# Performance work log

Hardware: AMD Instinct MI355X
Metric: run time of the kernel (lower is better)

## Reference

```python
import jax, jax.numpy as jnp
import numpy as np
from jax import lax

NHEAD = 8
EPS = 1e-5
B, T, DIN, DOUT = 32, 64, 512, 128
FF_ENC, FF_DEC, NLAYERS = 64, 16, 4


def _ln(x, g, b):
    mu = jnp.mean(x, -1, keepdims=True)
    var = jnp.mean(jnp.square(x - mu), -1, keepdims=True)
    return (x - mu) * lax.rsqrt(var + EPS) * g + b


def _lin(x, w, b):
    return x @ w.T + b


def _mha(q_in, kv_in, qkv_w, qkv_b, out_w, out_b):
    # PyTorch MultiheadAttention (batch_first, eval mode -> no dropout)
    b_, sq, d = q_in.shape
    sk = kv_in.shape[1]
    dh = d // NHEAD
    wq, wk, wv = jnp.split(qkv_w, 3, axis=0)
    bq, bk, bv = jnp.split(qkv_b, 3, axis=0)
    q = _lin(q_in, wq, bq).reshape(b_, sq, NHEAD, dh)
    k = _lin(kv_in, wk, bk).reshape(b_, sk, NHEAD, dh)
    v = _lin(kv_in, wv, bv).reshape(b_, sk, NHEAD, dh)
    s = jnp.einsum('bqhd,bkhd->bhqk', q, k) * (1.0 / np.sqrt(dh))
    a = jax.nn.softmax(s, axis=-1)
    o = jnp.einsum('bhqk,bkhd->bqhd', a, v).reshape(b_, sq, d)
    return _lin(o, out_w, out_b)


def _enc_layer(x, p):
    (qkv_w, qkv_b, ow, ob, f1w, f1b, f2w, f2b, g1, b1, g2, b2) = p
    # post-norm (norm_first=False), relu activation, dropout off (eval)
    x = _ln(x + _mha(x, x, qkv_w, qkv_b, ow, ob), g1, b1)
    ff = _lin(jax.nn.relu(_lin(x, f1w, f1b)), f2w, f2b)
    return _ln(x + ff, g2, b2)


def _dec_layer(tgt, mem, dp):
    (sqkv_w, sqkv_b, sow, sob, cqkv_w, cqkv_b, cow, cob,
     f1w, f1b, f2w, f2b, g1, b1, g2, b2, g3, b3) = dp
    x = _ln(tgt + _mha(tgt, tgt, sqkv_w, sqkv_b, sow, sob), g1, b1)  # no mask, as in source
    x = _ln(x + _mha(x, mem, cqkv_w, cqkv_b, cow, cob), g2, b2)
    ff = _lin(jax.nn.relu(_lin(x, f1w, f1b)), f2w, f2b)
    return _ln(x + ff, g3, b3)


def _forward(src, enc_qkv_w, enc_qkv_b, enc_out_w, enc_out_b,
             enc_ff1_w, enc_ff1_b, enc_ff2_w, enc_ff2_b,
             enc_ln1_g, enc_ln1_b, enc_ln2_g, enc_ln2_b,
             fc_w, fc_b,
             dec_sa_qkv_w, dec_sa_qkv_b, dec_sa_out_w, dec_sa_out_b,
             dec_ca_qkv_w, dec_ca_qkv_b, dec_ca_out_w, dec_ca_out_b,
             dec_ff1_w, dec_ff1_b, dec_ff2_w, dec_ff2_b,
             dec_ln1_g, dec_ln1_b, dec_ln2_g, dec_ln2_b, dec_ln3_g, dec_ln3_b):
    mem = src
    for i in range(NLAYERS):
        p = (enc_qkv_w[i], enc_qkv_b[i], enc_out_w[i], enc_out_b[i],
             enc_ff1_w[i], enc_ff1_b[i], enc_ff2_w[i], enc_ff2_b[i],
             enc_ln1_g[i], enc_ln1_b[i], enc_ln2_g[i], enc_ln2_b[i])
        mem = _enc_layer(mem, p)
    mem = _lin(mem, fc_w, fc_b)  # [B, T, DOUT]
    dp = (dec_sa_qkv_w, dec_sa_qkv_b, dec_sa_out_w, dec_sa_out_b,
          dec_ca_qkv_w, dec_ca_qkv_b, dec_ca_out_w, dec_ca_out_b,
          dec_ff1_w, dec_ff1_b, dec_ff2_w, dec_ff2_b,
          dec_ln1_g, dec_ln1_b, dec_ln2_g, dec_ln2_b, dec_ln3_g, dec_ln3_b)

    def step(tgt, t):
        out = _dec_layer(tgt, mem, dp)           # full decoder pass over padded tgt
        row = lax.dynamic_slice_in_dim(out, t, 1, axis=1)
        tgt = lax.dynamic_update_slice_in_dim(tgt, row, t + 1, axis=1)
        return tgt, None

    tgt0 = jnp.zeros((src.shape[0], T + 1, DOUT), src.dtype)
    tgt, _ = lax.scan(step, tgt0, jnp.arange(T))
    return tgt[:, 1:]


def setup_inputs() -> dict:
    key = jax.random.key(0)
    ks = iter(jax.random.split(key, 64))
    w = lambda *s: jax.random.normal(next(ks), s, jnp.float32) * 0.02
    z = lambda *s: jnp.zeros(s, jnp.float32)
    o = lambda *s: jnp.ones(s, jnp.float32)
    d = {}
    d['src'] = jax.random.normal(next(ks), (B, T, DIN), jnp.float32)
    d['enc_qkv_w'] = w(NLAYERS, 3 * DIN, DIN)
    d['enc_qkv_b'] = z(NLAYERS, 3 * DIN)
    d['enc_out_w'] = w(NLAYERS, DIN, DIN)
    d['enc_out_b'] = z(NLAYERS, DIN)
    d['enc_ff1_w'] = w(NLAYERS, FF_ENC, DIN)
    d['enc_ff1_b'] = z(NLAYERS, FF_ENC)
    d['enc_ff2_w'] = w(NLAYERS, DIN, FF_ENC)
    d['enc_ff2_b'] = z(NLAYERS, DIN)
    d['enc_ln1_g'] = o(NLAYERS, DIN)
    d['enc_ln1_b'] = z(NLAYERS, DIN)
    d['enc_ln2_g'] = o(NLAYERS, DIN)
    d['enc_ln2_b'] = z(NLAYERS, DIN)
    d['fc_w'] = w(DOUT, DIN)
    d['fc_b'] = z(DOUT)
    d['dec_sa_qkv_w'] = w(3 * DOUT, DOUT)
    d['dec_sa_qkv_b'] = z(3 * DOUT)
    d['dec_sa_out_w'] = w(DOUT, DOUT)
    d['dec_sa_out_b'] = z(DOUT)
    d['dec_ca_qkv_w'] = w(3 * DOUT, DOUT)
    d['dec_ca_qkv_b'] = z(3 * DOUT)
    d['dec_ca_out_w'] = w(DOUT, DOUT)
    d['dec_ca_out_b'] = z(DOUT)
    d['dec_ff1_w'] = w(FF_DEC, DOUT)
    d['dec_ff1_b'] = z(FF_DEC)
    d['dec_ff2_w'] = w(DOUT, FF_DEC)
    d['dec_ff2_b'] = z(DOUT)
    d['dec_ln1_g'] = o(DOUT)
    d['dec_ln1_b'] = z(DOUT)
    d['dec_ln2_g'] = o(DOUT)
    d['dec_ln2_b'] = z(DOUT)
    d['dec_ln3_g'] = o(DOUT)
    d['dec_ln3_b'] = z(DOUT)
    return d


def reference(src, enc_qkv_w, enc_qkv_b, enc_out_w, enc_out_b,
              enc_ff1_w, enc_ff1_b, enc_ff2_w, enc_ff2_b,
              enc_ln1_g, enc_ln1_b, enc_ln2_g, enc_ln2_b,
              fc_w, fc_b,
              dec_sa_qkv_w, dec_sa_qkv_b, dec_sa_out_w, dec_sa_out_b,
              dec_ca_qkv_w, dec_ca_qkv_b, dec_ca_out_w, dec_ca_out_b,
              dec_ff1_w, dec_ff1_b, dec_ff2_w, dec_ff2_b,
              dec_ln1_g, dec_ln1_b, dec_ln2_g, dec_ln2_b, dec_ln3_g, dec_ln3_b):
    return _forward(src, enc_qkv_w, enc_qkv_b, enc_out_w, enc_out_b,
                    enc_ff1_w, enc_ff1_b, enc_ff2_w, enc_ff2_b,
                    enc_ln1_g, enc_ln1_b, enc_ln2_g, enc_ln2_b,
                    fc_w, fc_b,
                    dec_sa_qkv_w, dec_sa_qkv_b, dec_sa_out_w, dec_sa_out_b,
                    dec_ca_qkv_w, dec_ca_qkv_b, dec_ca_out_w, dec_ca_out_b,
                    dec_ff1_w, dec_ff1_b, dec_ff2_w, dec_ff2_b,
                    dec_ln1_g, dec_ln1_b, dec_ln2_g, dec_ln2_b, dec_ln3_g, dec_ln3_b)
```

## Files before the change

kernel.cpp:

```cpp
#include <hip/hip_runtime.h>
#include <hip/hip_bf16.h>


typedef __attribute__((ext_vector_type(8))) short bf16x8;
typedef __attribute__((ext_vector_type(4))) float f32x4;
typedef __attribute__((ext_vector_type(4))) unsigned int u32x4;
typedef unsigned short ushort_t;
typedef unsigned int uint_t;

#define LN_EPS 1e-5f
#define KC_STRIDE 136
#define VT_STRIDE 72
#define SC_STRIDE 72

__device__ __forceinline__ ushort_t f2bfbits(float f){
  union { __hip_bfloat16 h; ushort_t u; } cv;
  cv.h = __float2bfloat16(f);
  return cv.u;
}
__device__ __forceinline__ uint_t pack2(float a, float b){
  return (uint_t)f2bfbits(a) | ((uint_t)f2bfbits(b) << 16);
}
__device__ __forceinline__ bf16x8 pack8(f32x4 u, f32x4 v){
  bf16x8 r;
  r[0]=(short)f2bfbits(u.x); r[1]=(short)f2bfbits(u.y);
  r[2]=(short)f2bfbits(u.z); r[3]=(short)f2bfbits(u.w);
  r[4]=(short)f2bfbits(v.x); r[5]=(short)f2bfbits(v.y);
  r[6]=(short)f2bfbits(v.z); r[7]=(short)f2bfbits(v.w);
  return r;
}

__global__ void __launch_bounds__(256) cvt10(
    const float* s0, ushort_t* d0, int n0,
    const float* s1, ushort_t* d1, int n1,
    const float* s2, ushort_t* d2, int n2,
    const float* s3, ushort_t* d3, int n3,
    const float* s4, ushort_t* d4, int n4,
    const float* s5, ushort_t* d5, int n5,
    const float* s6, ushort_t* d6, int n6,
    const float* s7, ushort_t* d7, int n7,
    const float* s8, ushort_t* d8, int n8,
    const float* s9, ushort_t* d9, int n9)
{
  const float* s; ushort_t* d; int n;
  switch (blockIdx.y){
    case 0: s=s0; d=d0; n=n0; break;
    case 1: s=s1; d=d1; n=n1; break;
    case 2: s=s2; d=d2; n=n2; break;
    case 3: s=s3; d=d3; n=n3; break;
    case 4: s=s4; d=d4; n=n4; break;
    case 5: s=s5; d=d5; n=n5; break;
    case 6: s=s6; d=d6; n=n6; break;
    case 7: s=s7; d=d7; n=n7; break;
    case 8: s=s8; d=d8; n=n8; break;
    default: s=s9; d=d9; n=n9; break;
  }
  for (int i = (blockIdx.x*256 + threadIdx.x)*8; i < n; i += gridDim.x*256*8){
    f32x4 u = *(const f32x4*)(s + i);
    f32x4 v = *(const f32x4*)(s + i + 4);
    u32x4 w;
    w[0]=pack2(u.x,u.y); w[1]=pack2(u.z,u.w); w[2]=pack2(v.x,v.y); w[3]=pack2(v.z,v.w);
    *(u32x4*)(d + i) = w;
  }
}

__global__ void __launch_bounds__(256) gemm_bf16(
    const ushort_t* __restrict__ A, const ushort_t* __restrict__ W,
    const float* __restrict__ bias, const float* __restrict__ resid,
    float* __restrict__ C, ushort_t* __restrict__ Cb,
    int M, int N, int K, int relu)
{
  const int tid  = threadIdx.x;
  const int lane = tid & 63;
  const int wid  = tid >> 6;
  const int rowBase = blockIdx.x * 64 + (wid >> 1) * 32;
  const int colBase = blockIdx.y * 64 + (wid & 1) * 32;
  const int r16 = lane & 15;
  const int kg  = lane >> 4;

  f32x4 zz = {0.f,0.f,0.f,0.f};
  f32x4 acc[2][2];
  acc[0][0]=zz; acc[0][1]=zz; acc[1][0]=zz; acc[1][1]=zz;

  const ushort_t* Ap = A + (size_t)(rowBase + r16) * K + kg*8;
  const ushort_t* Wp = W + (size_t)(colBase + r16) * K + kg*8;
  #pragma unroll 4
  for (int k0 = 0; k0 < K; k0 += 32){
    bf16x8 af0 = *(const bf16x8*)(Ap + k0);
    bf16x8 af1 = *(const bf16x8*)(Ap + (size_t)16*K + k0);
    bf16x8 bf0 = *(const bf16x8*)(Wp + k0);
    bf16x8 bf1 = *(const bf16x8*)(Wp + (size_t)16*K + k0);
    acc[0][0] = __builtin_amdgcn_mfma_f32_16x16x32_bf16(af0, bf0, acc[0][0], 0,0,0);
    acc[0][1] = __builtin_amdgcn_mfma_f32_16x16x32_bf16(af0, bf1, acc[0][1], 0,0,0);
    acc[1][0] = __builtin_amdgcn_mfma_f32_16x16x32_bf16(af1, bf0, acc[1][0], 0,0,0);
    acc[1][1] = __builtin_amdgcn_mfma_f32_16x16x32_bf16(af1, bf1, acc[1][1], 0,0,0);
  }

  #pragma unroll
  for (int mt = 0; mt < 2; ++mt)
  #pragma unroll
  for (int nt = 0; nt < 2; ++nt)
  #pragma unroll
  for (int i = 0; i < 4; ++i){
    int row = rowBase + mt*16 + kg*4 + i;
    int col = colBase + nt*16 + r16;
    float v = acc[mt][nt][i] + bias[col];
    if (resid) v += resid[(size_t)row * N + col];
    if (relu)  v = fmaxf(v, 0.f);
    if (C)  C[(size_t)row * N + col] = v;
    if (Cb) Cb[(size_t)row * N + col] = f2bfbits(v);
  }
}

#define APAD 68
__global__ void __launch_bounds__(256) enc_attn_kernel(
    const ushort_t* __restrict__ QKVb, ushort_t* __restrict__ Ob)
{
  __shared__ __attribute__((aligned(16))) float Qs[64][APAD];
  __shared__ __attribute__((aligned(16))) float Ks[64][APAD];
  __shared__ __attribute__((aligned(16))) float Vs[64][APAD];
  __shared__ __attribute__((aligned(16))) float Ss[64][APAD];
  const int b = blockIdx.x, h = blockIdx.y;
  const int tid = threadIdx.x;
  const ushort_t* base = QKVb + (size_t)b * 64 * 1536 + h * 64;
  for (int idx = tid; idx < 1536; idx += 256){
    int a = idx >> 9, rem = idx & 511;
    int tt = rem >> 3, c8 = (rem & 7) * 8;
    u32x4 w = *(const u32x4*)(base + (size_t)tt * 1536 + a * 512 + c8);
    float* dst = (a == 0) ? &Qs[tt][c8] : (a == 1) ? &Ks[tt][c8] : &Vs[tt][c8];
    #pragma unroll
    for (int j2 = 0; j2 < 4; ++j2){
      dst[2*j2]   = __uint_as_float(w[j2] << 16);
      dst[2*j2+1] = __uint_as_float(w[j2] & 0xffff0000u);
    }
  }
  __syncthreads();
  const int r = tid >> 2, cg = tid & 3;
  float qr[64];
  #pragma unroll
  for (int k4 = 0; k4 < 16; ++k4) *(f32x4*)&qr[k4*4] = *(const f32x4*)&Qs[r][k4*4];
  float sv[16];
  #pragma unroll
  for (int i = 0; i < 16; ++i){
    int c = cg * 16 + i;
    float acc = 0.f;
    #pragma unroll
    for (int k4 = 0; k4 < 16; ++k4){
      f32x4 kv = *(const f32x4*)&Ks[c][k4*4];
      acc += qr[k4*4+0]*kv.x + qr[k4*4+1]*kv.y + qr[k4*4+2]*kv.z + qr[k4*4+3]*kv.w;
    }
    sv[i] = acc * 0.125f;
  }
  float mx = -1e30f;
  #pragma unroll
  for (int i = 0; i < 16; ++i) mx = fmaxf(mx, sv[i]);
  mx = fmaxf(mx, __shfl_xor(mx, 1));
  mx = fmaxf(mx, __shfl_xor(mx, 2));
  float sum = 0.f;
  #pragma unroll
  for (int i = 0; i < 16; ++i){ sv[i] = __expf(sv[i] - mx); sum += sv[i]; }
  sum += __shfl_xor(sum, 1);
  sum += __shfl_xor(sum, 2);
  float inv = 1.f / sum;
  #pragma unroll
  for (int i = 0; i < 16; ++i) Ss[r][cg*16 + i] = sv[i] * inv;
  __syncthreads();
  float ar[64];
  #pragma unroll
  for (int k4 = 0; k4 < 16; ++k4) *(f32x4*)&ar[k4*4] = *(const f32x4*)&Ss[r][k4*4];
  f32x4 zz = {0.f,0.f,0.f,0.f};
  f32x4 o4[4]; o4[0]=zz; o4[1]=zz; o4[2]=zz; o4[3]=zz;
  for (int k = 0; k < 64; ++k){
    float s = ar[k];
    #pragma unroll
    for (int q = 0; q < 4; ++q){
      f32x4 v = *(const f32x4*)&Vs[k][cg*16 + q*4];
      o4[q] += v * s;
    }
  }
  ushort_t* op = Ob + ((size_t)(b * 64 + r)) * 512 + h * 64 + cg * 16;
  #pragma unroll
  for (int q = 0; q < 4; ++q){
    op[q*4+0] = f2bfbits(o4[q].x);
    op[q*4+1] = f2bfbits(o4[q].y);
    op[q*4+2] = f2bfbits(o4[q].z);
    op[q*4+3] = f2bfbits(o4[q].w);
  }
}

__global__ void __launch_bounds__(256) ln512_kernel(const float* __restrict__ R,
    const float* __restrict__ g, const float* __restrict__ bb,
    float* __restrict__ X, ushort_t* __restrict__ Xb)
{
  const int row  = blockIdx.x * 4 + (threadIdx.x >> 6);
  const int lane = threadIdx.x & 63;
  const float* p = R + (size_t)row * 512 + lane * 8;
  f32x4 u = *(const f32x4*)p;
  f32x4 v = *(const f32x4*)(p + 4);
  float s  = u.x+u.y+u.z+u.w + v.x+v.y+v.z+v.w;
  float sq = u.x*u.x+u.y*u.y+u.z*u.z+u.w*u.w + v.x*v.x+v.y*v.y+v.z*v.z+v.w*v.w;
  #pragma unroll
  for (int off = 1; off < 64; off <<= 1){
    s  += __shfl_xor(s, off);
    sq += __shfl_xor(sq, off);
  }
  float mu   = s  * (1.f/512.f);
  float var  = sq * (1.f/512.f) - mu*mu;
  float rstd = rsqrtf(var + LN_EPS);
  const float* gp = g  + lane * 8;
  const float* bp = bb + lane * 8;
  f32x4 g0 = *(const f32x4*)gp, g1v = *(const f32x4*)(gp+4);
  f32x4 b0 = *(const f32x4*)bp, b1v = *(const f32x4*)(bp+4);
  f32x4 o0, o1;
  o0.x=(u.x-mu)*rstd*g0.x+b0.x;  o0.y=(u.y-mu)*rstd*g0.y+b0.y;
  o0.z=(u.z-mu)*rstd*g0.z+b0.z;  o0.w=(u.w-mu)*rstd*g0.w+b0.w;
  o1.x=(v.x-mu)*rstd*g1v.x+b1v.x; o1.y=(v.y-mu)*rstd*g1v.y+b1v.y;
  o1.z=(v.z-mu)*rstd*g1v.z+b1v.z; o1.w=(v.w-mu)*rstd*g1v.w+b1v.w;
  float* xp = X + (size_t)row * 512 + lane * 8;
  *(f32x4*)xp       = o0;
  *(f32x4*)(xp + 4) = o1;
  u32x4 w;
  w[0]=pack2(o0.x,o0.y); w[1]=pack2(o0.z,o0.w); w[2]=pack2(o1.x,o1.y); w[3]=pack2(o1.z,o1.w);
  *(u32x4*)(Xb + (size_t)row * 512 + lane * 8) = w;
}

__device__ __forceinline__ void make_vec_bfrag(const float* __restrict__ x,
                                               int lane, bf16x8 bf[4]){
  const int kg = lane >> 4;
  const bool act = (lane & 15) == 0;
  bf16x8 z8 = {0,0,0,0,0,0,0,0};
  #pragma unroll
  for (int kb = 0; kb < 4; ++kb){
    f32x4 u = *(const f32x4*)(x + kb*32 + kg*8);
    f32x4 v = *(const f32x4*)(x + kb*32 + kg*8 + 4);
    bf16x8 r = pack8(u, v);
    bf[kb] = act ? r : z8;
  }
}

__global__ void __launch_bounds__(512) decode_kernel(
    const ushort_t* __restrict__ MEMb,
    const ushort_t* __restrict__ Wsaqkv,
    const ushort_t* __restrict__ Wsaout,
    const ushort_t* __restrict__ Wcaqkv,
    const ushort_t* __restrict__ Wcaout,
    const ushort_t* __restrict__ Wff1,
    const ushort_t* __restrict__ Wff2,
    const float* __restrict__ saqkv_b, const float* __restrict__ saout_b,
    const float* __restrict__ caqkv_b, const float* __restrict__ caout_b,
    const float* __restrict__ f1b, const float* __restrict__ f2b,
    const float* __restrict__ g1, const float* __restrict__ b1,
    const float* __restrict__ g2, const float* __restrict__ b2,
    const float* __restrict__ g3, const float* __restrict__ b3,
    float* __restrict__ Out)
{
  __shared__ __attribute__((aligned(16))) ushort_t Ksa[64*KC_STRIDE];
  __shared__ __attribute__((aligned(16))) ushort_t VsaT[128*VT_STRIDE];
  __shared__ __attribute__((aligned(16))) ushort_t Kc [64*KC_STRIDE];
  __shared__ __attribute__((aligned(16))) ushort_t VcT[128*VT_STRIDE];
  __shared__ __attribute__((aligned(16))) float scores[8*SC_STRIDE];
  __shared__ __attribute__((aligned(16))) float pbuf[8*SC_STRIDE];
  __shared__ __attribute__((aligned(16))) float xcur[128], x1[128], x2[128];
  __shared__ __attribute__((aligned(16))) float qbuf[128], obuf[128], rtmp[128];
  __shared__ __attribute__((aligned(16))) float hbuf[32];
  __shared__ __attribute__((aligned(16))) float bsaq[384];
  __shared__ __attribute__((aligned(16))) float bsao[128], bcaq[128], bcakv[256], bcao[128];
  __shared__ __attribute__((aligned(16))) float bff1[16], bff2[128];
  __shared__ __attribute__((aligned(16))) float lg1[128], lb1[128], lg2[128], lb2[128], lg3[128], lb3[128];

  const int tid  = threadIdx.x;
  const int lane = tid & 63;
  const int wid  = tid >> 6;
  const int col = lane & 15, kg = lane >> 4;
  const int b = blockIdx.x;
  f32x4 z4 = {0.f,0.f,0.f,0.f};
  bf16x8 z8 = {0,0,0,0,0,0,0,0};

  if (tid < 384) bsaq[tid] = saqkv_b[tid];
  if (tid < 256) bcakv[tid] = caqkv_b[128 + tid];
  if (tid < 128){
    bsao[tid] = saout_b[tid]; bcaq[tid] = caqkv_b[tid]; bcao[tid] = caout_b[tid]; bff2[tid] = f2b[tid];
    lg1[tid]=g1[tid]; lb1[tid]=b1[tid]; lg2[tid]=g2[tid]; lb2[tid]=b2[tid]; lg3[tid]=g3[tid]; lb3[tid]=b3[tid];
    xcur[tid] = 0.f;
  }
  if (tid < 16) bff1[tid] = f1b[tid];
  if (tid < 32) hbuf[tid] = 0.f;
  for (int i = tid; i < 128*VT_STRIDE; i += 512) VsaT[i] = 0;

  bf16x8 wsaq[3][4];
  #pragma unroll
  for (int r = 0; r < 3; ++r)
    #pragma unroll
    for (int kb = 0; kb < 4; ++kb)
      wsaq[r][kb] = *(const bf16x8*)(Wsaqkv + ((wid*3 + r)*16 + col)*128 + kb*32 + kg*8);
  bf16x8 wsao[4], wcaqr[4], wcaor[4], wf1[4];
  #pragma unroll
  for (int kb = 0; kb < 4; ++kb){
    wsao[kb]  = *(const bf16x8*)(Wsaout + (wid*16 + col)*128 + kb*32 + kg*8);
    wcaqr[kb] = *(const bf16x8*)(Wcaqkv + (wid*16 + col)*128 + kb*32 + kg*8);
    wcaor[kb] = *(const bf16x8*)(Wcaout + (wid*16 + col)*128 + kb*32 + kg*8);
    wf1[kb]   = *(const bf16x8*)(Wff1 + col*128 + kb*32 + kg*8);
  }
  bf16x8 wf2 = (kg < 2) ? *(const bf16x8*)(Wff2 + (wid*16 + col)*16 + kg*8) : z8;

  __syncthreads();

  {
    const ushort_t* Wkv = Wcaqkv + 128*128;
    const ushort_t* memb = MEMb + (size_t)b * 64 * 128;
    #pragma unroll
    for (int rr = 0; rr < 2; ++rr){
      int rt = wid*2 + rr;
      #pragma unroll
      for (int jt = 0; jt < 4; ++jt){
        f32x4 acc = z4;
        #pragma unroll
        for (int kb = 0; kb < 4; ++kb){
          bf16x8 a  = *(const bf16x8*)(Wkv  + (rt*16 + col)*128 + kb*32 + kg*8);
          bf16x8 bb = *(const bf16x8*)(memb + (size_t)(jt*16 + col)*128 + kb*32 + kg*8);
          acc = __builtin_amdgcn_mfma_f32_16x16x32_bf16(a, bb, acc, 0,0,0);
        }
        int j  = jt*16 + col;
        int r0 = rt*16 + kg*4;
        f32x4 o = acc + *(const f32x4*)(bcakv + r0);
        if (r0 < 128){
          ushort_t* p = Kc + j*KC_STRIDE + r0;
          p[0]=f2bfbits(o.x); p[1]=f2bfbits(o.y); p[2]=f2bfbits(o.z); p[3]=f2bfbits(o.w);
        } else {
          int d = r0 - 128;
          VcT[(d+0)*VT_STRIDE + j] = f2bfbits(o.x);
          VcT[(d+1)*VT_STRIDE + j] = f2bfbits(o.y);
          VcT[(d+2)*VT_STRIDE + j] = f2bfbits(o.z);
          VcT[(d+3)*VT_STRIDE + j] = f2bfbits(o.w);
        }
      }
    }
  }

  for (int t = 0; t < 64; ++t){
    __syncthreads();
    {
      bf16x8 xb[4];
      make_vec_bfrag(xcur, lane, xb);
      #pragma unroll
      for (int r = 0; r < 3; ++r){
        f32x4 acc = z4;
        #pragma unroll
        for (int kb = 0; kb < 4; ++kb)
          acc = __builtin_amdgcn_mfma_f32_16x16x32_bf16(wsaq[r][kb], xb[kb], acc, 0,0,0);
        if (col == 0){
          int r0 = (wid*3 + r)*16 + kg*4;
          f32x4 o = acc + *(const f32x4*)(bsaq + r0);
          if (r0 < 128){
            *(f32x4*)(qbuf + r0) = o;
          } else if (r0 < 256){
            ushort_t* p = Ksa + t*KC_STRIDE + (r0 - 128);
            p[0]=f2bfbits(o.x); p[1]=f2bfbits(o.y); p[2]=f2bfbits(o.z); p[3]=f2bfbits(o.w);
          } else {
            int d = r0 - 256;
            VsaT[(d+0)*VT_STRIDE + t] = f2bfbits(o.x);
            VsaT[(d+1)*VT_STRIDE + t] = f2bfbits(o.y);
            VsaT[(d+2)*VT_STRIDE + t] = f2bfbits(o.z);
            VsaT[(d+3)*VT_STRIDE + t] = f2bfbits(o.w);
          }
        }
      }
    }
    __syncthreads();
    if (wid < 4){
      const int jt = wid;
      const bool bval = (col == 0 && kg < 2) || (col == 1 && kg >= 2);
      #pragma unroll
      for (int hp = 0; hp < 4; ++hp){
        f32x4 u = *(const f32x4*)(qbuf + hp*32 + kg*8);
        f32x4 v = *(const f32x4*)(qbuf + hp*32 + kg*8 + 4);
        u *= 0.25f; v *= 0.25f;
        bf16x8 qb = pack8(u, v);
        qb = bval ? qb : z8;
        bf16x8 a = *(const bf16x8*)(Ksa + (jt*16 + col)*KC_STRIDE + hp*32 + kg*8);
        f32x4 d = __builtin_amdgcn_mfma_f32_16x16x32_bf16(a, qb, z4, 0,0,0);
        if (col < 2)
          *(f32x4*)(scores + (hp*2 + col)*SC_STRIDE + jt*16 + kg*4) = d;
      }
    }
    __syncthreads();
    if (wid == 0){
      const int h = lane >> 3, jj = lane & 7;
      float sv[8];
      *(f32x4*)(sv)     = *(const f32x4*)(scores + h*SC_STRIDE + jj*8);
      *(f32x4*)(sv + 4) = *(const f32x4*)(scores + h*SC_STRIDE + jj*8 + 4);
      #pragma unroll
      for (int i = 0; i < 8; ++i){ int j = jj*8 + i; sv[i] = (j <= t) ? sv[i] : -1e30f; }
      float mx = sv[0];
      #pragma unroll
      for (int i = 1; i < 8; ++i) mx = fmaxf(mx, sv[i]);
      mx = fmaxf(mx, __shfl_xor(mx, 1));
      mx = fmaxf(mx, __shfl_xor(mx, 2));
      mx = fmaxf(mx, __shfl_xor(mx, 4));
      float e[8];
      #pragma unroll
      for (int i = 0; i < 8; ++i) e[i] = __expf(sv[i] - mx);
      if (jj == 0) e[0] *= (float)(65 - t);
      float sum = 0.f;
      #pragma unroll
      for (int i = 0; i < 8; ++i) sum += e[i];
      sum += __shfl_xor(sum, 1);
      sum += __shfl_xor(sum, 2);
      sum += __shfl_xor(sum, 4);
      float inv = 1.f / sum;
      f32x4 p0 = {e[0]*inv, e[1]*inv, e[2]*inv, e[3]*inv};
      f32x4 p1 = {e[4]*inv, e[5]*inv, e[6]*inv, e[7]*inv};
      *(f32x4*)(pbuf + h*SC_STRIDE + jj*8)     = p0;
      *(f32x4*)(pbuf + h*SC_STRIDE + jj*8 + 4) = p1;
    }
    __syncthreads();
    {
      const int h = wid;
      f32x4 acc = z4;
      #pragma unroll
      for (int jb = 0; jb < 2; ++jb){
        f32x4 u = *(const f32x4*)(pbuf + h*SC_STRIDE + jb*32 + kg*8);
        f32x4 v = *(const f32x4*)(pbuf + h*SC_STRIDE + jb*32 + kg*8 + 4);
        bf16x8 pb = pack8(u, v);
        pb = (col == 0) ? pb : z8;
        bf16x8 a = *(const bf16x8*)(VsaT + (h*16 + col)*VT_STRIDE + jb*32 + kg*8);
        acc = __builtin_amdgcn_mfma_f32_16x16x32_bf16(a, pb, acc, 0,0,0);
      }
      if (col == 0)
        *(f32x4*)(obuf + h*16 + kg*4) = acc;
    }
    __syncthreads();
    {
      bf16x8 xb[4];
      make_vec_bfrag(obuf, lane, xb);
      f32x4 acc = z4;
      #pragma unroll
      for (int kb = 0; kb < 4; ++kb)
        acc = __builtin_amdgcn_mfma_f32_16x16x32_bf16(wsao[kb], xb[kb], acc, 0,0,0);
      if (col == 0){
        int r0 = wid*16 + kg*4;
        *(f32x4*)(rtmp + r0) = acc + *(const f32x4*)(bsao + r0);
      }
    }
    __syncthreads();
    if (wid == 0){
      float a0 = rtmp[lane] + xcur[lane];
      float a1 = rtmp[lane+64] + xcur[lane+64];
      float s = a0 + a1, sq = a0*a0 + a1*a1;
      #pragma unroll
      for (int off = 1; off < 64; off <<= 1){ s += __shfl_xor(s, off); sq += __shfl_xor(sq, off); }
      float mu = s*(1.f/128.f), var = sq*(1.f/128.f) - mu*mu;
      float rs = rsqrtf(var + LN_EPS);
      x1[lane]    = (a0-mu)*rs*lg1[lane]    + lb1[lane];
      x1[lane+64] = (a1-mu)*rs*lg1[lane+64] + lb1[lane+64];
    }
    __syncthreads();
    {
      bf16x8 xb[4];
      make_vec_bfrag(x1, lane, xb);
      f32x4 acc = z4;
      #pragma unroll
      for (int kb = 0; kb < 4; ++kb)
        acc = __builtin_amdgcn_mfma_f32_16x16x32_bf16(wcaqr[kb], xb[kb], acc, 0,0,0);
      if (col == 0){
        int r0 = wid*16 + kg*4;
        *(f32x4*)(qbuf + r0) = acc + *(const f32x4*)(bcaq + r0);
      }
    }
    __syncthreads();
    if (wid < 4){
      const int jt = wid;
      const bool bval = (col == 0 && kg < 2) || (col == 1 && kg >= 2);
      #pragma unroll
      for (int hp = 0; hp < 4; ++hp){
        f32x4 u = *(const f32x4*)(qbuf + hp*32 + kg*8);
        f32x4 v = *(const f32x4*)(qbuf + hp*32 + kg*8 + 4);
        u *= 0.25f; v *= 0.25f;
        bf16x8 qb = pack8(u, v);
        qb = bval ? qb : z8;
        bf16x8 a = *(const bf16x8*)(Kc + (jt*16 + col)*KC_STRIDE + hp*32 + kg*8);
        f32x4 d = __builtin_amdgcn_mfma_f32_16x16x32_bf16(a, qb, z4, 0,0,0);
        if (col < 2)
          *(f32x4*)(scores + (hp*2 + col)*SC_STRIDE + jt*16 + kg*4) = d;
      }
    }
    __syncthreads();
    if (wid == 0){
      const int h = lane >> 3, jj = lane & 7;
      float sv[8];
      *(f32x4*)(sv)     = *(const f32x4*)(scores + h*SC_STRIDE + jj*8);
      *(f32x4*)(sv + 4) = *(const f32x4*)(scores + h*SC_STRIDE + jj*8 + 4);
      float mx = sv[0];
      #pragma unroll
      for (int i = 1; i < 8; ++i) mx = fmaxf(mx, sv[i]);
      mx = fmaxf(mx, __shfl_xor(mx, 1));
      mx = fmaxf(mx, __shfl_xor(mx, 2));
      mx = fmaxf(mx, __shfl_xor(mx, 4));
      float e[8], sum = 0.f;
      #pragma unroll
      for (int i = 0; i < 8; ++i){ e[i] = __expf(sv[i] - mx); sum += e[i]; }
      sum += __shfl_xor(sum, 1);
      sum += __shfl_xor(sum, 2);
      sum += __shfl_xor(sum, 4);
      float inv = 1.f / sum;
      f32x4 p0 = {e[0]*inv, e[1]*inv, e[2]*inv, e[3]*inv};
      f32x4 p1 = {e[4]*inv, e[5]*inv, e[6]*inv, e[7]*inv};
      *(f32x4*)(pbuf + h*SC_STRIDE + jj*8)     = p0;
      *(f32x4*)(pbuf + h*SC_STRIDE + jj*8 + 4) = p1;
    }
    __syncthreads();
    {
      const int h = wid;
      f32x4 acc = z4;
      #pragma unroll
      for (int jb = 0; jb < 2; ++jb){
        f32x4 u = *(const f32x4*)(pbuf + h*SC_STRIDE + jb*32 + kg*8);
        f32x4 v = *(const f32x4*)(pbuf + h*SC_STRIDE + jb*32 + kg*8 + 4);
        bf16x8 pb = pack8(u, v);
        pb = (col == 0) ? pb : z8;
        bf16x8 a = *(const bf16x8*)(VcT + (h*16 + col)*VT_STRIDE + jb*32 + kg*8);
        acc = __builtin_amdgcn_mfma_f32_16x16x32_bf16(a, pb, acc, 0,0,0);
      }
      if (col == 0)
        *(f32x4*)(obuf + h*16 + kg*4) = acc;
    }
    __syncthreads();
    {
      bf16x8 xb[4];
      make_vec_bfrag(obuf, lane, xb);
      f32x4 acc = z4;
      #pragma unroll
      for (int kb = 0; kb < 4; ++kb)
        acc = __builtin_amdgcn_mfma_f32_16x16x32_bf16(wcaor[kb], xb[kb], acc, 0,0,0);
      if (col == 0){
        int r0 = wid*16 + kg*4;
        *(f32x4*)(rtmp + r0) = acc + *(const f32x4*)(bcao + r0);
      }
    }
    __syncthreads();
    if (wid == 0){
      float a0 = rtmp[lane] + x1[lane];
      float a1 = rtmp[lane+64] + x1[lane+64];
      float s = a0 + a1, sq = a0*a0 + a1*a1;
      #pragma unroll
      for (int off = 1; off < 64; off <<= 1){ s += __shfl_xor(s, off); sq += __shfl_xor(sq, off); }
      float mu = s*(1.f/128.f), var = sq*(1.f/128.f) - mu*mu;
      float rs = rsqrtf(var + LN_EPS);
      x2[lane]    = (a0-mu)*rs*lg2[lane]    + lb2[lane];
      x2[lane+64] = (a1-mu)*rs*lg2[lane+64] + lb2[lane+64];
    }
    __syncthreads();
    if (wid == 7){
      bf16x8 xb[4];
      make_vec_bfrag(x2, lane, xb);
      f32x4 acc = z4;
      #pragma unroll
      for (int kb = 0; kb < 4; ++kb)
        acc = __builtin_amdgcn_mfma_f32_16x16x32_bf16(wf1[kb], xb[kb], acc, 0,0,0);
      if (col == 0){
        int r0 = kg*4;
        f32x4 o = acc + *(const f32x4*)(bff1 + r0);
        hbuf[r0+0]=fmaxf(o.x,0.f); hbuf[r0+1]=fmaxf(o.y,0.f);
        hbuf[r0+2]=fmaxf(o.z,0.f); hbuf[r0+3]=fmaxf(o.w,0.f);
      }
    }
    __syncthreads();
    {
      f32x4 u = *(const f32x4*)(hbuf + kg*8);
      f32x4 v = *(const f32x4*)(hbuf + kg*8 + 4);
      bf16x8 hb = pack8(u, v);
      hb = (col == 0) ? hb : z8;
      f32x4 acc = __builtin_amdgcn_mfma_f32_16x16x32_bf16(wf2, hb, z4, 0,0,0);
      if (col == 0){
        int r0 = wid*16 + kg*4;
        *(f32x4*)(rtmp + r0) = acc + *(const f32x4*)(bff2 + r0);
      }
    }
    __syncthreads();
    if (wid == 0){
      float a0 = rtmp[lane] + x2[lane];
      float a1 = rtmp[lane+64] + x2[lane+64];
      float s = a0 + a1, sq = a0*a0 + a1*a1;
      #pragma unroll
      for (int off = 1; off < 64; off <<= 1){ s += __shfl_xor(s, off); sq += __shfl_xor(sq, off); }
      float mu = s*(1.f/128.f), var = sq*(1.f/128.f) - mu*mu;
      float rs = rsqrtf(var + LN_EPS);
      float o0 = (a0-mu)*rs*lg3[lane]    + lb3[lane];
      float o1 = (a1-mu)*rs*lg3[lane+64] + lb3[lane+64];
      xcur[lane]    = o0;
      xcur[lane+64] = o1;
      Out[((size_t)(b*64 + t))*128 + lane]      = o0;
      Out[((size_t)(b*64 + t))*128 + lane + 64] = o1;
    }
  }
}

extern "C" void kernel_launch(void* const* d_in, const int* in_sizes, int n_in,
                              void* d_out, int out_size, void* d_ws, size_t ws_size,
                              hipStream_t stream)
{
  (void)in_sizes; (void)n_in; (void)out_size; (void)ws_size;
  const float* src   = (const float*)d_in[0];
  const float* eqkvw = (const float*)d_in[1];
  const float* eqkvb = (const float*)d_in[2];
  const float* eow   = (const float*)d_in[3];
  const float* eob   = (const float*)d_in[4];
  const float* ef1w  = (const float*)d_in[5];
  const float* ef1b  = (const float*)d_in[6];
  const float* ef2w  = (const float*)d_in[7];
  const float* ef2b  = (const float*)d_in[8];
  const float* eg1   = (const float*)d_in[9];
  const float* eb1   = (const float*)d_in[10];
  const float* eg2   = (const float*)d_in[11];
  const float* eb2   = (const float*)d_in[12];
  const float* fcw   = (const float*)d_in[13];
  const float* fcb   = (const float*)d_in[14];
  const float* dsaqw = (const float*)d_in[15];
  const float* dsaqb = (const float*)d_in[16];
  const float* dsaow = (const float*)d_in[17];
  const float* dsaob = (const float*)d_in[18];
  const float* dcaqw = (const float*)d_in[19];
  const float* dcaqb = (const float*)d_in[20];
  const float* dcaow = (const float*)d_in[21];
  const float* dcaob = (const float*)d_in[22];
  const float* df1w  = (const float*)d_in[23];
  const float* df1b  = (const float*)d_in[24];
  const float* df2w  = (const float*)d_in[25];
  const float* df2b  = (const float*)d_in[26];
  const float* dg1   = (const float*)d_in[27];
  const float* db1   = (const float*)d_in[28];
  const float* dg2   = (const float*)d_in[29];
  const float* db2   = (const float*)d_in[30];
  const float* dg3   = (const float*)d_in[31];
  const float* db3   = (const float*)d_in[32];

  float* ws = (float*)d_ws;
  ushort_t* QKVb   = (ushort_t*)ws;
  float*    Rb     = ws;
  float*    XA     = ws + 1572864;
  float*    XB     = ws + 2621440;
  ushort_t* Xinb   = (ushort_t*)(ws + 3670016);
  ushort_t* Ob     = (ushort_t*)(ws + 4194304);
  ushort_t* XBb    = (ushort_t*)(ws + 4718592);
  ushort_t* Hb     = (ushort_t*)(ws + 5242880);
  ushort_t* MEMbb  = (ushort_t*)(ws + 5308416);
  ushort_t* eqkvw_l= (ushort_t*)(ws + 5439488);
  ushort_t* eow_l  = (ushort_t*)(ws + 5832704);
  ushort_t* ef1w_b = (ushort_t*)(ws + 5963776);
  ushort_t* ef2w_b = (ushort_t*)(ws + 6029312);
  ushort_t* fcw_b  = (ushort_t*)(ws + 6094848);
  ushort_t* dsaqw_b  = (ushort_t*)(ws + 6127616);
  ushort_t* dsaow_b  = (ushort_t*)(ws + 6152192);
  ushort_t* dcaqkv_b = (ushort_t*)(ws + 6160384);
  ushort_t* dcaow_b  = (ushort_t*)(ws + 6184960);
  ushort_t* df1w_b   = (ushort_t*)(ws + 6193152);
  ushort_t* df2w_b   = (ushort_t*)(ws + 6194176);

  cvt10<<<dim3(512,10),256,0,stream>>>(
      src,   Xinb,    1048576,
      ef1w,  ef1w_b,  131072,
      ef2w,  ef2w_b,  131072,
      fcw,   fcw_b,   65536,
      dsaqw, dsaqw_b, 49152,
      dsaow, dsaow_b, 16384,
      dcaqw, dcaqkv_b,49152,
      dcaow, dcaow_b, 16384,
      df1w,  df1w_b,  2048,
      df2w,  df2w_b,  2048);

  const float* Xres = src;
  for (int l = 0; l < 4; ++l){
    cvt10<<<dim3(384,2),256,0,stream>>>(
        eqkvw + (size_t)l*786432, eqkvw_l, 786432,
        eow   + (size_t)l*262144, eow_l,   262144,
        nullptr,nullptr,0, nullptr,nullptr,0, nullptr,nullptr,0,
        nullptr,nullptr,0, nullptr,nullptr,0, nullptr,nullptr,0,
        nullptr,nullptr,0, nullptr,nullptr,0);
    gemm_bf16<<<dim3(32,24),256,0,stream>>>(Xinb, eqkvw_l, eqkvb + l*1536, nullptr,
                                            nullptr, QKVb, 2048, 1536, 512, 0);
    enc_attn_kernel<<<dim3(32,8),256,0,stream>>>(QKVb, Ob);
    gemm_bf16<<<dim3(32,8),256,0,stream>>>(Ob, eow_l, eob + l*512, Xres,
                                           Rb, nullptr, 2048, 512, 512, 0);
    ln512_kernel<<<dim3(512),256,0,stream>>>(Rb, eg1 + l*512, eb1 + l*512, XB, XBb);
    gemm_bf16<<<dim3(32,1),256,0,stream>>>(XBb, ef1w_b + (size_t)l*32768, ef1b + l*64,
                                           nullptr, nullptr, Hb, 2048, 64, 512, 1);
    gemm_bf16<<<dim3(32,8),256,0,stream>>>(Hb, ef2w_b + (size_t)l*32768, ef2b + l*512,
                                           XB, Rb, nullptr, 2048, 512, 64, 0);
    ln512_kernel<<<dim3(512),256,0,stream>>>(Rb, eg2 + l*512, eb2 + l*512, XA, Xinb);
    Xres = XA;
  }
  gemm_bf16<<<dim3(32,2),256,0,stream>>>(Xinb, fcw_b, fcb, nullptr,
                                         nullptr, MEMbb, 2048, 128, 512, 0);
  decode_kernel<<<dim3(32),512,0,stream>>>(MEMbb,
      dsaqw_b, dsaow_b, dcaqkv_b, dcaow_b, df1w_b, df2w_b,
      dsaqb, dsaob, dcaqb, dcaob, df1b, df2b,
      dg1, db1, dg2, db2, dg3, db3, (float*)d_out);
}
```

Measured before the change: 841.8 us.

## Fuse out-projection and FFN with LayerNorm, hoist weight conversion out of loop

Replaces the out-projection GEMM plus LayerNorm pair and the FFN1/FFN2 GEMMs plus LayerNorm with two fused kernels. Each block computes 16 full rows with MFMA and does the row reduction in-block, so the fp32 residual buffer and the hidden activations no longer round-trip through global memory, and the launch count drops. When the workspace is large enough, all encoder layer weights are converted to bf16 in the single upfront conversion launch instead of once per layer. The fused kernels run only 128 blocks and read weights straight from global memory without LDS staging, which may lower occupancy and weight reuse compared with the tiled GEMM.

```diff
diff --git a/kernel.cpp b/kernel.cpp
--- a/kernel.cpp
+++ b/kernel.cpp
@@ -30,30 +30,28 @@
   return r;
 }
 
-__global__ void __launch_bounds__(256) cvt10(
-    const float* s0, ushort_t* d0, int n0,
-    const float* s1, ushort_t* d1, int n1,
-    const float* s2, ushort_t* d2, int n2,
-    const float* s3, ushort_t* d3, int n3,
-    const float* s4, ushort_t* d4, int n4,
-    const float* s5, ushort_t* d5, int n5,
-    const float* s6, ushort_t* d6, int n6,
-    const float* s7, ushort_t* d7, int n7,
-    const float* s8, ushort_t* d8, int n8,
-    const float* s9, ushort_t* d9, int n9)
+__global__ void __launch_bounds__(256) cvt12(
+    const float* s0, ushort_t* d0, int n0,  const float* s1, ushort_t* d1, int n1,
+    const float* s2, ushort_t* d2, int n2,  const float* s3, ushort_t* d3, int n3,
+    const float* s4, ushort_t* d4, int n4,  const float* s5, ushort_t* d5, int n5,
+    const float* s6, ushort_t* d6, int n6,  const float* s7, ushort_t* d7, int n7,
+    const float* s8, ushort_t* d8, int n8,  const float* s9, ushort_t* d9, int n9,
+    const float* sa, ushort_t* da, int na,  const float* sb, ushort_t* db, int nb)
 {
   const float* s; ushort_t* d; int n;
   switch (blockIdx.y){
-    case 0: s=s0; d=d0; n=n0; break;
-    case 1: s=s1; d=d1; n=n1; break;
-    case 2: s=s2; d=d2; n=n2; break;
-    case 3: s=s3; d=d3; n=n3; break;
-    case 4: s=s4; d=d4; n=n4; break;
-    case 5: s=s5; d=d5; n=n5; break;
-    case 6: s=s6; d=d6; n=n6; break;
-    case 7: s=s7; d=d7; n=n7; break;
-    case 8: s=s8; d=d8; n=n8; break;
-    default: s=s9; d=d9; n=n9; break;
+    case 0:  s=s0; d=d0; n=n0; break;
+    case 1:  s=s1; d=d1; n=n1; break;
+    case 2:  s=s2; d=d2; n=n2; break;
+    case 3:  s=s3; d=d3; n=n3; break;
+    case 4:  s=s4; d=d4; n=n4; break;
+    case 5:  s=s5; d=d5; n=n5; break;
+    case 6:  s=s6; d=d6; n=n6; break;
+    case 7:  s=s7; d=d7; n=n7; break;
+    case 8:  s=s8; d=d8; n=n8; break;
+    case 9:  s=s9; d=d9; n=n9; break;
+    case 10: s=sa; d=da; n=na; break;
+    default: s=sb; d=db; n=nb; break;
   }
   for (int i = (blockIdx.x*256 + threadIdx.x)*8; i < n; i += gridDim.x*256*8){
     f32x4 u = *(const f32x4*)(s + i);
@@ -188,40 +186,176 @@
   }
 }
 
-__global__ void __launch_bounds__(256) ln512_kernel(const float* __restrict__ R,
+__global__ void __launch_bounds__(256) oproj_ln(
+    const ushort_t* __restrict__ A, const ushort_t* __restrict__ W,
+    const float* __restrict__ bias, const float* __restrict__ resid,
     const float* __restrict__ g, const float* __restrict__ bb,
     float* __restrict__ X, ushort_t* __restrict__ Xb)
 {
-  const int row  = blockIdx.x * 4 + (threadIdx.x >> 6);
-  const int lane = threadIdx.x & 63;
-  const float* p = R + (size_t)row * 512 + lane * 8;
-  f32x4 u = *(const f32x4*)p;
-  f32x4 v = *(const f32x4*)(p + 4);
-  float s  = u.x+u.y+u.z+u.w + v.x+v.y+v.z+v.w;
-  float sq = u.x*u.x+u.y*u.y+u.z*u.z+u.w*u.w + v.x*v.x+v.y*v.y+v.z*v.z+v.w*v.w;
-  #pragma unroll
-  for (int off = 1; off < 64; off <<= 1){
-    s  += __shfl_xor(s, off);
-    sq += __shfl_xor(sq, off);
-  }
-  float mu   = s  * (1.f/512.f);
-  float var  = sq * (1.f/512.f) - mu*mu;
-  float rstd = rsqrtf(var + LN_EPS);
-  const float* gp = g  + lane * 8;
-  const float* bp = bb + lane * 8;
-  f32x4 g0 = *(const f32x4*)gp, g1v = *(const f32x4*)(gp+4);
-  f32x4 b0 = *(const f32x4*)bp, b1v = *(const f32x4*)(bp+4);
-  f32x4 o0, o1;
-  o0.x=(u.x-mu)*rstd*g0.x+b0.x;  o0.y=(u.y-mu)*rstd*g0.y+b0.y;
-  o0.z=(u.z-mu)*rstd*g0.z+b0.z;  o0.w=(u.w-mu)*rstd*g0.w+b0.w;
-  o1.x=(v.x-mu)*rstd*g1v.x+b1v.x; o1.y=(v.y-mu)*rstd*g1v.y+b1v.y;
-  o1.z=(v.z-mu)*rstd*g1v.z+b1v.z; o1.w=(v.w-mu)*rstd*g1v.w+b1v.w;
-  float* xp = X + (size_t)row * 512 + lane * 8;
-  *(f32x4*)xp       = o0;
-  *(f32x4*)(xp + 4) = o1;
-  u32x4 w;
-  w[0]=pack2(o0.x,o0.y); w[1]=pack2(o0.z,o0.w); w[2]=pack2(o1.x,o1.y); w[3]=pack2(o1.z,o1.w);
-  *(u32x4*)(Xb + (size_t)row * 512 + lane * 8) = w;
+  __shared__ float wsum[4][16], wsq[4][16];
+  __shared__ float mu_s[16], rs_s[16];
+  const int tid = threadIdx.x, lane = tid & 63, wid = tid >> 6;
+  const int c16 = lane & 15, kg = lane >> 4;
+  const int rowBase = blockIdx.x * 16;
+  f32x4 z4 = {0.f,0.f,0.f,0.f};
+  f32x4 acc[8];
+  #pragma unroll
+  for (int nt = 0; nt < 8; ++nt) acc[nt] = z4;
+
+  const ushort_t* Ap = A + (size_t)(rowBase + c16)*512 + kg*8;
+  const ushort_t* Wp = W + (size_t)(wid*128 + c16)*512 + kg*8;
+  #pragma unroll 2
+  for (int kb = 0; kb < 16; ++kb){
+    bf16x8 af = *(const bf16x8*)(Ap + kb*32);
+    #pragma unroll
+    for (int nt = 0; nt < 8; ++nt){
+      bf16x8 wf = *(const bf16x8*)(Wp + (size_t)nt*16*512 + kb*32);
+      acc[nt] = __builtin_amdgcn_mfma_f32_16x16x32_bf16(af, wf, acc[nt], 0,0,0);
+    }
+  }
+  float ps[4] = {0,0,0,0}, pq[4] = {0,0,0,0};
+  #pragma unroll
+  for (int nt = 0; nt < 8; ++nt){
+    int coln = wid*128 + nt*16 + c16;
+    float bcol = bias[coln];
+    #pragma unroll
+    for (int i = 0; i < 4; ++i){
+      int row = rowBase + kg*4 + i;
+      float v = acc[nt][i] + bcol + resid[(size_t)row*512 + coln];
+      acc[nt][i] = v;
+      ps[i] += v; pq[i] += v*v;
+    }
+  }
+  #pragma unroll
+  for (int off = 1; off < 16; off <<= 1){
+    #pragma unroll
+    for (int i = 0; i < 4; ++i){
+      ps[i] += __shfl_xor(ps[i], off);
+      pq[i] += __shfl_xor(pq[i], off);
+    }
+  }
+  if (c16 == 0){
+    #pragma unroll
+    for (int i = 0; i < 4; ++i){ wsum[wid][kg*4+i] = ps[i]; wsq[wid][kg*4+i] = pq[i]; }
+  }
+  __syncthreads();
+  if (tid < 16){
+    float s = wsum[0][tid]+wsum[1][tid]+wsum[2][tid]+wsum[3][tid];
+    float q = wsq[0][tid]+wsq[1][tid]+wsq[2][tid]+wsq[3][tid];
+    float mu = s * (1.f/512.f);
+    float var = q * (1.f/512.f) - mu*mu;
+    mu_s[tid] = mu; rs_s[tid] = rsqrtf(var + LN_EPS);
+  }
+  __syncthreads();
+  #pragma unroll
+  for (int nt = 0; nt < 8; ++nt){
+    int coln = wid*128 + nt*16 + c16;
+    float gg = g[coln], b2 = bb[coln];
+    #pragma unroll
+    for (int i = 0; i < 4; ++i){
+      int r = kg*4 + i;
+      int row = rowBase + r;
+      float o = (acc[nt][i] - mu_s[r]) * rs_s[r] * gg + b2;
+      X[(size_t)row*512 + coln] = o;
+      Xb[(size_t)row*512 + coln] = f2bfbits(o);
+    }
+  }
+}
+
+__global__ void __launch_bounds__(256) ff_ln(
+    const ushort_t* __restrict__ A,
+    const ushort_t* __restrict__ W1,
+    const float* __restrict__ b1v,
+    const ushort_t* __restrict__ W2,
+    const float* __restrict__ b2v,
+    const float* __restrict__ resid,
+    const float* __restrict__ g, const float* __restrict__ bb,
+    float* __restrict__ X, ushort_t* __restrict__ Xb)
+{
+  __shared__ ushort_t hsh[16][72];
+  __shared__ float wsum[4][16], wsq[4][16];
+  __shared__ float mu_s[16], rs_s[16];
+  const int tid = threadIdx.x, lane = tid & 63, wid = tid >> 6;
+  const int c16 = lane & 15, kg = lane >> 4;
+  const int rowBase = blockIdx.x * 16;
+  f32x4 z4 = {0.f,0.f,0.f,0.f};
+
+  {
+    f32x4 acch = z4;
+    const ushort_t* Ap  = A  + (size_t)(rowBase + c16)*512 + kg*8;
+    const ushort_t* W1p = W1 + (size_t)(wid*16 + c16)*512 + kg*8;
+    #pragma unroll 4
+    for (int kb = 0; kb < 16; ++kb){
+      bf16x8 af = *(const bf16x8*)(Ap + kb*32);
+      bf16x8 wf = *(const bf16x8*)(W1p + kb*32);
+      acch = __builtin_amdgcn_mfma_f32_16x16x32_bf16(af, wf, acch, 0,0,0);
+    }
+    float bc = b1v[wid*16 + c16];
+    #pragma unroll
+    for (int i = 0; i < 4; ++i)
+      hsh[kg*4 + i][wid*16 + c16] = f2bfbits(fmaxf(acch[i] + bc, 0.f));
+  }
+  __syncthreads();
+
+  f32x4 acc[8];
+  #pragma unroll
+  for (int nt = 0; nt < 8; ++nt) acc[nt] = z4;
+  #pragma unroll
+  for (int kb = 0; kb < 2; ++kb){
+    bf16x8 af = *(const bf16x8*)&hsh[c16][kg*8 + kb*32];
+    #pragma unroll
+    for (int nt = 0; nt < 8; ++nt){
+      bf16x8 wf = *(const bf16x8*)(W2 + (size_t)(wid*128 + nt*16 + c16)*64 + kg*8 + kb*32);
+      acc[nt] = __builtin_amdgcn_mfma_f32_16x16x32_bf16(af, wf, acc[nt], 0,0,0);
+    }
+  }
+  float ps[4] = {0,0,0,0}, pq[4] = {0,0,0,0};
+  #pragma unroll
+  for (int nt = 0; nt < 8; ++nt){
+    int coln = wid*128 + nt*16 + c16;
+    float bcol = b2v[coln];
+    #pragma unroll
+    for (int i = 0; i < 4; ++i){
+      int row = rowBase + kg*4 + i;
+      float v = acc[nt][i] + bcol + resid[(size_t)row*512 + coln];
+      acc[nt][i] = v;
+      ps[i] += v; pq[i] += v*v;
+    }
+  }
+  #pragma unroll
+  for (int off = 1; off < 16; off <<= 1){
+    #pragma unroll
+    for (int i = 0; i < 4; ++i){
+      ps[i] += __shfl_xor(ps[i], off);
+      pq[i] += __shfl_xor(pq[i], off);
+    }
+  }
+  if (c16 == 0){
+    #pragma unroll
+    for (int i = 0; i < 4; ++i){ wsum[wid][kg*4+i] = ps[i]; wsq[wid][kg*4+i] = pq[i]; }
+  }
+  __syncthreads();
+  if (tid < 16){
+    float s = wsum[0][tid]+wsum[1][tid]+wsum[2][tid]+wsum[3][tid];
+    float q = wsq[0][tid]+wsq[1][tid]+wsq[2][tid]+wsq[3][tid];
+    float mu = s * (1.f/512.f);
+    float var = q * (1.f/512.f) - mu*mu;
+    mu_s[tid] = mu; rs_s[tid] = rsqrtf(var + LN_EPS);
+  }
+  __syncthreads();
+  #pragma unroll
+  for (int nt = 0; nt < 8; ++nt){
+    int coln = wid*128 + nt*16 + c16;
+    float gg = g[coln], b2c = bb[coln];
+    #pragma unroll
+    for (int i = 0; i < 4; ++i){
+      int r = kg*4 + i;
+      int row = rowBase + r;
+      float o = (acc[nt][i] - mu_s[r]) * rs_s[r] * gg + b2c;
+      X[(size_t)row*512 + coln] = o;
+      Xb[(size_t)row*512 + coln] = f2bfbits(o);
+    }
+  }
 }
 
 __device__ __forceinline__ void make_vec_bfrag(const float* __restrict__ x,
@@ -240,12 +374,9 @@
 
 __global__ void __launch_bounds__(512) decode_kernel(
     const ushort_t* __restrict__ MEMb,
-    const ushort_t* __restrict__ Wsaqkv,
-    const ushort_t* __restrict__ Wsaout,
-    const ushort_t* __restrict__ Wcaqkv,
-    const ushort_t* __restrict__ Wcaout,
-    const ushort_t* __restrict__ Wff1,
-    const ushort_t* __restrict__ Wff2,
+    const ushort_t* __restrict__ Wsaqkv, const ushort_t* __restrict__ Wsaout,
+    const ushort_t* __restrict__ Wcaqkv, const ushort_t* __restrict__ Wcaout,
+    const ushort_t* __restrict__ Wff1, const ushort_t* __restrict__ Wff2,
     const float* __restrict__ saqkv_b, const float* __restrict__ saout_b,
     const float* __restrict__ caqkv_b, const float* __restrict__ caout_b,
     const float* __restrict__ f1b, const float* __restrict__ f2b,
@@ -599,7 +730,7 @@
                               void* d_out, int out_size, void* d_ws, size_t ws_size,
                               hipStream_t stream)
 {
-  (void)in_sizes; (void)n_in; (void)out_size; (void)ws_size;
+  (void)in_sizes; (void)n_in; (void)out_size;
   const float* src   = (const float*)d_in[0];
   const float* eqkvw = (const float*)d_in[1];
   const float* eqkvb = (const float*)d_in[2];
@@ -636,28 +767,33 @@
 
   float* ws = (float*)d_ws;
   ushort_t* QKVb   = (ushort_t*)ws;
-  float*    Rb     = ws;
   float*    XA     = ws + 1572864;
   float*    XB     = ws + 2621440;
   ushort_t* Xinb   = (ushort_t*)(ws + 3670016);
   ushort_t* Ob     = (ushort_t*)(ws + 4194304);
   ushort_t* XBb    = (ushort_t*)(ws + 4718592);
-  ushort_t* Hb     = (ushort_t*)(ws + 5242880);
-  ushort_t* MEMbb  = (ushort_t*)(ws + 5308416);
-  ushort_t* eqkvw_l= (ushort_t*)(ws + 5439488);
-  ushort_t* eow_l  = (ushort_t*)(ws + 5832704);
-  ushort_t* ef1w_b = (ushort_t*)(ws + 5963776);
-  ushort_t* ef2w_b = (ushort_t*)(ws + 6029312);
-  ushort_t* fcw_b  = (ushort_t*)(ws + 6094848);
-  ushort_t* dsaqw_b  = (ushort_t*)(ws + 6127616);
-  ushort_t* dsaow_b  = (ushort_t*)(ws + 6152192);
-  ushort_t* dcaqkv_b = (ushort_t*)(ws + 6160384);
-  ushort_t* dcaow_b  = (ushort_t*)(ws + 6184960);
-  ushort_t* df1w_b   = (ushort_t*)(ws + 6193152);
-  ushort_t* df2w_b   = (ushort_t*)(ws + 6194176);
-
-  cvt10<<<dim3(512,10),256,0,stream>>>(
+  ushort_t* MEMbb  = (ushort_t*)(ws + 5242880);
+
+  const bool big = ws_size >= (size_t)7702560 * 4;
+  size_t off = 5373952;
+  ushort_t* eqkvw_b = (ushort_t*)(ws + off);
+  off += big ? 1572864 : 393216;
+  ushort_t* eow_b   = (ushort_t*)(ws + off);
+  off += big ? 524288 : 131072;
+  ushort_t* ef1w_b  = (ushort_t*)(ws + off); off += 65536;
+  ushort_t* ef2w_b  = (ushort_t*)(ws + off); off += 65536;
+  ushort_t* fcw_b   = (ushort_t*)(ws + off); off += 32768;
+  ushort_t* dsaqw_b = (ushort_t*)(ws + off); off += 24576;
+  ushort_t* dsaow_b = (ushort_t*)(ws + off); off += 8192;
+  ushort_t* dcaqkv_b= (ushort_t*)(ws + off); off += 24576;
+  ushort_t* dcaow_b = (ushort_t*)(ws + off); off += 8192;
+  ushort_t* df1w_b  = (ushort_t*)(ws + off); off += 1024;
+  ushort_t* df2w_b  = (ushort_t*)(ws + off); off += 1056;
+
+  cvt12<<<dim3(768,12),256,0,stream>>>(
       src,   Xinb,    1048576,
+      big ? eqkvw : nullptr, big ? eqkvw_b : nullptr, big ? 3145728 : 0,
+      big ? eow   : nullptr, big ? eow_b   : nullptr, big ? 1048576 : 0,
       ef1w,  ef1w_b,  131072,
       ef2w,  ef2w_b,  131072,
       fcw,   fcw_b,   65536,
@@ -670,23 +806,30 @@
 
   const float* Xres = src;
   for (int l = 0; l < 4; ++l){
-    cvt10<<<dim3(384,2),256,0,stream>>>(
-        eqkvw + (size_t)l*786432, eqkvw_l, 786432,
-        eow   + (size_t)l*262144, eow_l,   262144,
-        nullptr,nullptr,0, nullptr,nullptr,0, nullptr,nullptr,0,
-        nullptr,nullptr,0, nullptr,nullptr,0, nullptr,nullptr,0,
-        nullptr,nullptr,0, nullptr,nullptr,0);
-    gemm_bf16<<<dim3(32,24),256,0,stream>>>(Xinb, eqkvw_l, eqkvb + l*1536, nullptr,
+    const ushort_t* wq;
+    const ushort_t* wo;
+    if (big){
+      wq = eqkvw_b + (size_t)l*786432;
+      wo = eow_b   + (size_t)l*262144;
+    } else {
+      cvt12<<<dim3(768,2),256,0,stream>>>(
+          eqkvw + (size_t)l*786432, eqkvw_b, 786432,
+          eow   + (size_t)l*262144, eow_b,   262144,
+          nullptr,nullptr,0, nullptr,nullptr,0, nullptr,nullptr,0,
+          nullptr,nullptr,0, nullptr,nullptr,0, nullptr,nullptr,0,
+          nullptr,nullptr,0, nullptr,nullptr,0, nullptr,nullptr,0,
+          nullptr,nullptr,0);
+      wq = eqkvw_b;
+      wo = eow_b;
+    }
+    gemm_bf16<<<dim3(32,24),256,0,stream>>>(Xinb, wq, eqkvb + l*1536, nullptr,
                                             nullptr, QKVb, 2048, 1536, 512, 0);
     enc_attn_kernel<<<dim3(32,8),256,0,stream>>>(QKVb, Ob);
-    gemm_bf16<<<dim3(32,8),256,0,stream>>>(Ob, eow_l, eob + l*512, Xres,
-                                           Rb, nullptr, 2048, 512, 512, 0);
-    ln512_kernel<<<dim3(512),256,0,stream>>>(Rb, eg1 + l*512, eb1 + l*512, XB, XBb);
-    gemm_bf16<<<dim3(32,1),256,0,stream>>>(XBb, ef1w_b + (size_t)l*32768, ef1b + l*64,
-                                           nullptr, nullptr, Hb, 2048, 64, 512, 1);
-    gemm_bf16<<<dim3(32,8),256,0,stream>>>(Hb, ef2w_b + (size_t)l*32768, ef2b + l*512,
-                                           XB, Rb, nullptr, 2048, 512, 64, 0);
-    ln512_kernel<<<dim3(512),256,0,stream>>>(Rb, eg2 + l*512, eb2 + l*512, XA, Xinb);
+    oproj_ln<<<dim3(128),256,0,stream>>>(Ob, wo, eob + l*512, Xres,
+                                         eg1 + l*512, eb1 + l*512, XB, XBb);
+    ff_ln<<<dim3(128),256,0,stream>>>(XBb, ef1w_b + (size_t)l*32768, ef1b + l*64,
+                                      ef2w_b + (size_t)l*32768, ef2b + l*512,
+                                      XB, eg2 + l*512, eb2 + l*512, XA, Xinb);
     Xres = XA;
   }
   gemm_bf16<<<dim3(32,2),256,0,stream>>>(Xinb, fcw_b, fcb, nullptr,
```

Measured after the change: 834.7 us. No clear change (-0.8%).
